# Kernel tuning notes

Measured on AMD Instinct MI355X. Metric: run time of the kernel, lower is better.

Reference implementation:

```python
import jax, jax.numpy as jnp
import numpy as np

B, S, H, NH, L = 8, 512, 768, 12, 12
D = H // NH
EPS = 1e-12


def setup_inputs() -> dict:
    key = jax.random.key(0)
    ks = jax.random.split(key, 16)
    sc = 0.02
    inp = {
        "x": jax.random.normal(ks[0], (B, S, H), dtype=jnp.float32),
        # stacked per-layer params, leading dim L
        "Wq": jax.random.normal(ks[1], (L, H, H), dtype=jnp.float32) * sc,
        "bq": jnp.zeros((L, H), dtype=jnp.float32),
        "Wk": jax.random.normal(ks[2], (L, H, H), dtype=jnp.float32) * sc,
        "bk": jnp.zeros((L, H), dtype=jnp.float32),
        "Wv": jax.random.normal(ks[3], (L, H, H), dtype=jnp.float32) * sc,
        "bv": jnp.zeros((L, H), dtype=jnp.float32),
        "Wo": jax.random.normal(ks[4], (L, H, H), dtype=jnp.float32) * sc,
        "bo": jnp.zeros((L, H), dtype=jnp.float32),
        "ln1_g": jnp.ones((L, H), dtype=jnp.float32),
        "ln1_b": jnp.zeros((L, H), dtype=jnp.float32),
        # NOTE: original code applies pff2 (hidden->hidden, relu) TWICE; pff1 is unused.
        "W2": jax.random.normal(ks[5], (L, H, H), dtype=jnp.float32) * sc,
        "b2": jnp.zeros((L, H), dtype=jnp.float32),
        "ln2_g": jnp.ones((L, H), dtype=jnp.float32),
        "ln2_b": jnp.zeros((L, H), dtype=jnp.float32),
    }
    return inp


def _layernorm(x, g, b):
    m = jnp.mean(x, axis=-1, keepdims=True)
    v = jnp.mean(jnp.square(x - m), axis=-1, keepdims=True)
    return (x - m) * jax.lax.rsqrt(v + EPS) * g + b


def _block(x, p):
    (Wq, bq, Wk, bk, Wv, bv, Wo, bo, g1, be1, W2, b2, g2, be2) = p
    # projections: [B,S,H] -> [B,NH,S,D]
    def split(t):
        return t.reshape(B, S, NH, D).transpose(0, 2, 1, 3)
    q = split(x @ Wq + bq)
    k = split(x @ Wk + bk)
    v = split(x @ Wv + bv)
    scores = jnp.einsum("bhqd,bhkd->bhqk", q, k) / jnp.sqrt(jnp.float32(D))
    att = jax.nn.softmax(scores, axis=-1)  # no mask: original passes mask into `training` slot
    ctx = jnp.einsum("bhqk,bhkd->bhqd", att, v)
    ctx = ctx.transpose(0, 2, 1, 3).reshape(B, S, H)
    attn_out = ctx @ Wo + bo
    out1 = _layernorm(x + attn_out, g1, be1)
    # faithful bug replication: pff2 applied twice, pff1 unused
    h = jax.nn.relu(out1 @ W2 + b2)
    h = jax.nn.relu(h @ W2 + b2)
    out2 = _layernorm(out1 + h, g2, be2)
    return out2


def reference(x, Wq, bq, Wk, bk, Wv, bv, Wo, bo, ln1_g, ln1_b, W2, b2, ln2_g, ln2_b):
    params = (Wq, bq, Wk, bk, Wv, bv, Wo, bo, ln1_g, ln1_b, W2, b2, ln2_g, ln2_b)

    def step(carry, p):
        return _block(carry, p), None

    out, _ = jax.lax.scan(step, x, params)
    return out
```

## Files before the change

kernel.cpp:

```cpp
#include <hip/hip_runtime.h>
#include <cstdint>

typedef __bf16 bf16;
typedef __attribute__((ext_vector_type(4))) __bf16 bf16x4;
typedef __attribute__((ext_vector_type(8))) __bf16 bf16x8;
typedef __attribute__((ext_vector_type(4))) float f32x4;

#define ASYNC16(gptr, lptr)                                                      \
  __builtin_amdgcn_global_load_lds(                                              \
      (const __attribute__((address_space(1))) unsigned int*)(gptr),             \
      (__attribute__((address_space(3))) unsigned int*)(lptr), 16, 0, 0)

template <int BM, int BN, bool BIAS, bool RELU, int RESMODE, bool OUTB, bool VTOUT>
__global__ __launch_bounds__(256) void gemm_bt(
    const bf16* __restrict__ A, const bf16* __restrict__ B, void* __restrict__ C,
    const float* __restrict__ bias, const float* __restrict__ res,
    bf16* __restrict__ vt, int K,
    int lda, int ldb, int ldc, int bdiv, long sA1, long sA2, long sB1, long sB2,
    long sC1, long sC2, float scale)
{
  constexpr int FM = BM / 32, FN = BN / 32;
  constexpr int CALLS_A = BM / 64, CALLS_B = BN / 64;
  __shared__ __align__(16) bf16 As[2 * BM * 32];
  __shared__ __align__(16) bf16 Bs[2 * BN * 32];
  const int tid = threadIdx.x;
  const int wave = tid >> 6, lane = tid & 63;
  const int zb = blockIdx.z / bdiv, zh = blockIdx.z % bdiv;
  const bf16* Ab = A + zb * sA1 + zh * sA2 + (long)blockIdx.y * BM * lda;
  const bf16* Bb = B + zb * sB1 + zh * sB2 + (long)blockIdx.x * BN * ldb;
  const int rA = lane >> 2, kA = (lane & 3) * 8;
  const int wm = wave >> 1, wn = wave & 1;
  const int mBase = wm * (BM / 2) + (lane & 15);
  const int nBase = wn * (BN / 2) + (lane & 15);
  const int kOff = (lane >> 4) * 8;

  f32x4 acc[FM][FN] = {};

  for (int k0 = 0; k0 < K; k0 += 64) {
#pragma unroll
    for (int hh = 0; hh < 2; ++hh) {
      const int kh = k0 + hh * 32;
#pragma unroll
      for (int c = 0; c < CALLS_A; ++c) {
        const int cb = (wave * CALLS_A + c) << 10;
        ASYNC16(Ab + (long)((cb >> 6) + rA) * lda + kh + kA,
                ((char*)As) + hh * (BM * 64) + cb);
      }
#pragma unroll
      for (int c = 0; c < CALLS_B; ++c) {
        const int cb = (wave * CALLS_B + c) << 10;
        ASYNC16(Bb + (long)((cb >> 6) + rA) * ldb + kh + kA,
                ((char*)Bs) + hh * (BN * 64) + cb);
      }
    }
    __syncthreads();
#pragma unroll
    for (int t = 0; t < 2; ++t) {
      const bf16* Asub = As + t * BM * 32;
      const bf16* Bsub = Bs + t * BN * 32;
      bf16x8 af[FM], bfr[FN];
#pragma unroll
      for (int i = 0; i < FM; ++i)
        af[i] = *(const bf16x8*)&Asub[(mBase + i * 16) * 32 + kOff];
#pragma unroll
      for (int j = 0; j < FN; ++j)
        bfr[j] = *(const bf16x8*)&Bsub[(nBase + j * 16) * 32 + kOff];
#pragma unroll
      for (int i = 0; i < FM; ++i)
#pragma unroll
        for (int j = 0; j < FN; ++j)
          acc[i][j] = __builtin_amdgcn_mfma_f32_16x16x32_bf16(af[i], bfr[j], acc[i][j], 0, 0, 0);
    }
    __syncthreads();
  }

  const long cBase = zb * sC1 + zh * sC2;
  const int rowB = blockIdx.y * BM + wm * (BM / 2) + ((lane >> 4) << 2);
  const int colB = blockIdx.x * BN + wn * (BN / 2) + (lane & 15);
#pragma unroll
  for (int i = 0; i < FM; ++i) {
    const int row0 = rowB + i * 16;
#pragma unroll
    for (int j = 0; j < FN; ++j) {
      const int col = colB + j * 16;
      float bv = 0.f;
      if constexpr (BIAS) bv = bias[col];
      bf16x4 pk;
#pragma unroll
      for (int r = 0; r < 4; ++r) {
        const int row = row0 + r;
        float v = acc[i][j][r] * scale + bv;
        if constexpr (RELU) v = fmaxf(v, 0.f);
        const long idx = cBase + (long)row * ldc + col;
        if constexpr (RESMODE == 1) v += res[idx];
        if constexpr (OUTB) ((bf16*)C)[idx] = (bf16)v;
        else                ((float*)C)[idx] = v;
        if constexpr (VTOUT) pk[r] = (bf16)v;
      }
      if constexpr (VTOUT) {
        if (col >= 1536) {
          const int cc = col - 1536;
          const int h = cc >> 6, d = cc & 63;
          const int b = row0 >> 9, s = row0 & 511;
          *(bf16x4*)&vt[(((long)(b * 12 + h) * 64 + d) << 9) + s] = pk;
        }
      }
    }
  }
}

__global__ __launch_bounds__(512, 1) void fattn(
    const bf16* __restrict__ qkv, const bf16* __restrict__ vT,
    bf16* __restrict__ ctx)
{
  __shared__ __align__(16) bf16 Qs[64 * 64];
  __shared__ __align__(16) bf16 KVs[512 * 64];
  __shared__ __align__(16) bf16 Ps[64 * 520];
  __shared__ float sm[64 * 4];
  __shared__ float ssum[64 * 4];

  const int tid = threadIdx.x, wave = tid >> 6, lane = tid & 63;
  const int wg = wave >> 2, wc = wave & 3;
  const int bh = blockIdx.y;
  const int b = bh / 12, h = bh % 12;
  const int q0 = blockIdx.x * 64;
  const bf16* Qg = qkv + (long)(b * 512 + q0) * 2304 + h * 64;
  const bf16* Kg = qkv + (long)(b * 512) * 2304 + 768 + h * 64;
  const bf16* Vg = vT + (long)bh * 32768;

  const int rq = lane >> 3;
  const int kx = (((lane & 7) ^ rq) << 3);
  ASYNC16(Qg + (long)(wave * 8 + rq) * 2304 + kx, ((char*)Qs) + (wave << 10));
#pragma unroll
  for (int c = 0; c < 8; ++c) {
    const int cb = (wave * 8 + c) << 10;
    ASYNC16(Kg + (long)((cb >> 7) + rq) * 2304 + kx, ((char*)KVs) + cb);
  }
  __syncthreads();

  const int m0 = lane & 15, q = lane >> 4;
  const int sw = (m0 & 7);
  f32x4 acc[2][8] = {};
#pragma unroll
  for (int t = 0; t < 2; ++t) {
    const int ch = ((t * 4 + q) ^ sw) << 3;
    bf16x8 af[2];
#pragma unroll
    for (int i = 0; i < 2; ++i)
      af[i] = *(const bf16x8*)&Qs[(wg * 32 + i * 16 + m0) * 64 + ch];
#pragma unroll
    for (int j = 0; j < 8; ++j) {
      bf16x8 bf = *(const bf16x8*)&KVs[(wc * 128 + j * 16 + m0) * 64 + ch];
#pragma unroll
      for (int i = 0; i < 2; ++i)
        acc[i][j] = __builtin_amdgcn_mfma_f32_16x16x32_bf16(af[i], bf, acc[i][j], 0, 0, 0);
    }
  }

#pragma unroll
  for (int i = 0; i < 2; ++i)
#pragma unroll
    for (int r = 0; r < 4; ++r) {
      float m = acc[i][0][r];
#pragma unroll
      for (int j = 1; j < 8; ++j) m = fmaxf(m, acc[i][j][r]);
#pragma unroll
      for (int msk = 1; msk < 16; msk <<= 1) m = fmaxf(m, __shfl_xor(m, msk));
      if (m0 == 0) sm[(wg * 32 + i * 16 + q * 4 + r) * 4 + wc] = m;
    }
  __syncthreads();

  {
#pragma unroll
    for (int c = 0; c < 8; ++c) {
      const int d = wave * 8 + c;
      const int cb = (wave * 8 + c) << 10;
      ASYNC16(Vg + (long)d * 512 + ((lane ^ c) << 3), ((char*)KVs) + cb);
    }
  }

  const float SCL = 0.125f;
#pragma unroll
  for (int i = 0; i < 2; ++i)
#pragma unroll
    for (int r = 0; r < 4; ++r) {
      const int row = wg * 32 + i * 16 + q * 4 + r;
      f32x4 mv = *(const f32x4*)&sm[row * 4];
      const float M = fmaxf(fmaxf(mv[0], mv[1]), fmaxf(mv[2], mv[3])) * SCL;
      float s = 0.f;
#pragma unroll
      for (int j = 0; j < 8; ++j) {
        const float p = __expf(acc[i][j][r] * SCL - M);
        s += p;
        Ps[row * 520 + wc * 128 + j * 16 + m0] = (bf16)p;
      }
#pragma unroll
      for (int msk = 1; msk < 16; msk <<= 1) s += __shfl_xor(s, msk);
      if (m0 == 0) ssum[row * 4 + wc] = s;
    }
  __syncthreads();

  f32x4 cacc[2] = {};
#pragma unroll
  for (int t = 0; t < 16; ++t) {
    const int ch = ((t * 4 + q) ^ sw) << 3;
    bf16x8 bf = *(const bf16x8*)&KVs[(wc * 16 + m0) * 512 + ch];
#pragma unroll
    for (int i = 0; i < 2; ++i) {
      bf16x8 af = *(const bf16x8*)&Ps[(wg * 32 + i * 16 + m0) * 520 + t * 32 + q * 8];
      cacc[i] = __builtin_amdgcn_mfma_f32_16x16x32_bf16(af, bf, cacc[i], 0, 0, 0);
    }
  }
  const long cbase = (long)(b * 512 + q0) * 768 + h * 64;
  const int col = wc * 16 + m0;
#pragma unroll
  for (int i = 0; i < 2; ++i)
#pragma unroll
    for (int r = 0; r < 4; ++r) {
      const int row = wg * 32 + i * 16 + q * 4 + r;
      f32x4 sv = *(const f32x4*)&ssum[row * 4];
      const float inv = 1.f / (sv[0] + sv[1] + sv[2] + sv[3]);
      ctx[cbase + (long)row * 768 + col] = (bf16)(cacc[i][r] * inv);
    }
}

__global__ __launch_bounds__(256) void wprep(
    const float* __restrict__ Wq, const float* __restrict__ Wk,
    const float* __restrict__ Wv, const float* __restrict__ Wo,
    const float* __restrict__ W2, bf16* __restrict__ Tqkv, bf16* __restrict__ To,
    bf16* __restrict__ T2)
{
  const int l = blockIdx.z / 5, t = blockIdx.z % 5;
  const int k0 = blockIdx.x * 64, n0 = blockIdx.y * 64;
  const float* W = (t == 0) ? Wq : (t == 1) ? Wk : (t == 2) ? Wv : (t == 3) ? Wo : W2;
  W += (long)l * 589824;
  __shared__ __align__(16) bf16 tile[64][72];
  const int tid = threadIdx.x;
  const int r = tid >> 2, c = (tid & 3) * 16;
  const float* src = W + (long)(k0 + r) * 768 + n0 + c;
  bf16x8 s0, s1;
#pragma unroll
  for (int i = 0; i < 2; ++i) {
    f32x4 v0 = *(const f32x4*)(src + i * 8);
    f32x4 v1 = *(const f32x4*)(src + i * 8 + 4);
    bf16x8& dstv = i ? s1 : s0;
#pragma unroll
    for (int qq = 0; qq < 4; ++qq) { dstv[qq] = (bf16)v0[qq]; dstv[qq + 4] = (bf16)v1[qq]; }
  }
  *(bf16x8*)&tile[r][c] = s0;
  *(bf16x8*)&tile[r][c + 8] = s1;
  __syncthreads();
  bf16x8 o0, o1;
#pragma unroll
  for (int i = 0; i < 8; ++i) { o0[i] = tile[c + i][r]; o1[i] = tile[c + 8 + i][r]; }
  bf16* dst;
  if (t < 3)       dst = Tqkv + (long)l * 2304 * 768 + (long)(t * 768 + n0 + r) * 768 + k0 + c;
  else if (t == 3) dst = To + (long)l * 589824 + (long)(n0 + r) * 768 + k0 + c;
  else             dst = T2 + (long)l * 589824 + (long)(n0 + r) * 768 + k0 + c;
  *(bf16x8*)dst = o0;
  *(bf16x8*)(dst + 8) = o1;
}

__global__ void bias_concat(const float* __restrict__ bq, const float* __restrict__ bk,
                            const float* __restrict__ bv, float* __restrict__ o)
{
  const int i = blockIdx.x * 256 + threadIdx.x;
  if (i >= 12 * 2304) return;
  const int l = i / 2304, n = i % 2304;
  o[i] = (n < 768) ? bq[l * 768 + n] : (n < 1536) ? bk[l * 768 + n - 768] : bv[l * 768 + n - 1536];
}

__global__ void xconv(const float* __restrict__ x, float* __restrict__ xf, bf16* __restrict__ xb)
{
  const long i = (long)blockIdx.x * 256 + threadIdx.x;
  const float v = x[i];
  xf[i] = v;
  xb[i] = (bf16)v;
}

__global__ __launch_bounds__(256) void layernorm_k(
    const float* __restrict__ in, const float* __restrict__ g,
    const float* __restrict__ b, float* __restrict__ outf, bf16* __restrict__ outb)
{
  const long row = blockIdx.x;
  const int tid = threadIdx.x;
  const float* xr = in + row * 768;
  const float v0 = xr[tid], v1 = xr[tid + 256], v2 = xr[tid + 512];
  float s = v0 + v1 + v2;
  float qv = v0 * v0 + v1 * v1 + v2 * v2;
#pragma unroll
  for (int o = 32; o > 0; o >>= 1) { s += __shfl_down(s, o); qv += __shfl_down(qv, o); }
  __shared__ float rs[4], rq[4];
  const int wave = tid >> 6, lane = tid & 63;
  if (lane == 0) { rs[wave] = s; rq[wave] = qv; }
  __syncthreads();
  const float st = rs[0] + rs[1] + rs[2] + rs[3];
  const float qt = rq[0] + rq[1] + rq[2] + rq[3];
  const float mean = st * (1.f / 768.f);
  float var = qt * (1.f / 768.f) - mean * mean;
  var = fmaxf(var, 0.f);
  const float rstd = rsqrtf(var + 1e-12f);
  const float y0 = (v0 - mean) * rstd * g[tid] + b[tid];
  const float y1 = (v1 - mean) * rstd * g[tid + 256] + b[tid + 256];
  const float y2 = (v2 - mean) * rstd * g[tid + 512] + b[tid + 512];
  float* of = outf + row * 768;
  bf16* ob = outb + row * 768;
  of[tid] = y0;        of[tid + 256] = y1;        of[tid + 512] = y2;
  ob[tid] = (bf16)y0;  ob[tid + 256] = (bf16)y1;  ob[tid + 512] = (bf16)y2;
}

extern "C" void kernel_launch(void* const* d_in, const int* in_sizes, int n_in,
                              void* d_out, int out_size, void* d_ws, size_t ws_size,
                              hipStream_t stream)
{
  const float* x   = (const float*)d_in[0];
  const float* Wq  = (const float*)d_in[1];
  const float* bq  = (const float*)d_in[2];
  const float* Wk  = (const float*)d_in[3];
  const float* bk  = (const float*)d_in[4];
  const float* Wv  = (const float*)d_in[5];
  const float* bv  = (const float*)d_in[6];
  const float* Wo  = (const float*)d_in[7];
  const float* bo  = (const float*)d_in[8];
  const float* g1  = (const float*)d_in[9];
  const float* be1 = (const float*)d_in[10];
  const float* W2  = (const float*)d_in[11];
  const float* b2  = (const float*)d_in[12];
  const float* g2  = (const float*)d_in[13];
  const float* be2 = (const float*)d_in[14];
  (void)in_sizes; (void)n_in; (void)out_size; (void)ws_size;

  char* ws = (char*)d_ws;
  size_t off = 0;
  auto alloc = [&](size_t bytes) {
    void* p = ws + off;
    off = (off + bytes + 255) & ~(size_t)255;
    return p;
  };
  bf16*  wTqkv = (bf16*)alloc(12L * 2304 * 768 * 2);
  bf16*  wTo   = (bf16*)alloc(12L * 768 * 768 * 2);
  bf16*  wT2   = (bf16*)alloc(12L * 768 * 768 * 2);
  float* bqkv  = (float*)alloc(12L * 2304 * 4);
  float* xf    = (float*)alloc(4096L * 768 * 4);
  bf16*  xb    = (bf16*)alloc(4096L * 768 * 2);
  bf16*  qkv   = (bf16*)alloc(4096L * 2304 * 2);
  bf16*  vT    = (bf16*)alloc(96L * 64 * 512 * 2);
  bf16*  ctx   = (bf16*)alloc(4096L * 768 * 2);
  float* res1  = (float*)alloc(4096L * 768 * 4);
  float* out1f = (float*)alloc(4096L * 768 * 4);
  bf16*  out1b = (bf16*)alloc(4096L * 768 * 2);
  bf16*  h1b   = (bf16*)alloc(4096L * 768 * 2);
  float* res2  = (float*)alloc(4096L * 768 * 4);

  wprep<<<dim3(12, 12, 60), 256, 0, stream>>>(Wq, Wk, Wv, Wo, W2, wTqkv, wTo, wT2);
  bias_concat<<<dim3(108), 256, 0, stream>>>(bq, bk, bv, bqkv);
  xconv<<<dim3(12288), 256, 0, stream>>>(x, xf, xb);

  for (int l = 0; l < 12; ++l) {
    const bf16* wq_l   = wTqkv + (long)l * 2304 * 768;
    const bf16* wo_l   = wTo + (long)l * 589824;
    const bf16* w2_l   = wT2 + (long)l * 589824;
    const float* bqk_l = bqkv + l * 2304;
    float* lnout = (l == 11) ? (float*)d_out : xf;

    gemm_bt<128, 128, true, false, 0, true, true><<<dim3(18, 32, 1), 256, 0, stream>>>(
        xb, wq_l, qkv, bqk_l, nullptr, vT, 768, 768, 768, 2304,
        1, 0, 0, 0, 0, 0, 0, 1.f);
    fattn<<<dim3(8, 96), 512, 0, stream>>>(qkv, vT, ctx);
    gemm_bt<128, 64, true, false, 1, false, false><<<dim3(12, 32, 1), 256, 0, stream>>>(
        ctx, wo_l, res1, bo + l * 768, xf, nullptr, 768, 768, 768, 768,
        1, 0, 0, 0, 0, 0, 0, 1.f);
    layernorm_k<<<dim3(4096), 256, 0, stream>>>(res1, g1 + l * 768, be1 + l * 768, out1f, out1b);
    gemm_bt<128, 64, true, true, 0, true, false><<<dim3(12, 32, 1), 256, 0, stream>>>(
        out1b, w2_l, h1b, b2 + l * 768, nullptr, nullptr, 768, 768, 768, 768,
        1, 0, 0, 0, 0, 0, 0, 1.f);
    gemm_bt<128, 64, true, true, 1, false, false><<<dim3(12, 32, 1), 256, 0, stream>>>(
        h1b, w2_l, res2, b2 + l * 768, out1f, nullptr, 768, 768, 768, 768,
        1, 0, 0, 0, 0, 0, 0, 1.f);
    layernorm_k<<<dim3(4096), 256, 0, stream>>>(res2, g2 + l * 768, be2 + l * 768, lnout, xb);
  }
}
```

Measured before the change: 1.728 ms.

## Recompute LayerNorm residual in GEMM epilogue from row stats; rewrite weight transpose

New measurement: 1.710 ms. No clear change (-1.0%).

```diff
diff --git a/kernel.cpp b/kernel.cpp
--- a/kernel.cpp
+++ b/kernel.cpp
@@ -5,6 +5,7 @@
 typedef __attribute__((ext_vector_type(4))) __bf16 bf16x4;
 typedef __attribute__((ext_vector_type(8))) __bf16 bf16x8;
 typedef __attribute__((ext_vector_type(4))) float f32x4;
+typedef __attribute__((ext_vector_type(2))) float f32x2;
 
 #define ASYNC16(gptr, lptr)                                                      \
   __builtin_amdgcn_global_load_lds(                                              \
@@ -15,7 +16,8 @@
 __global__ __launch_bounds__(256) void gemm_bt(
     const bf16* __restrict__ A, const bf16* __restrict__ B, void* __restrict__ C,
     const float* __restrict__ bias, const float* __restrict__ res,
-    bf16* __restrict__ vt, int K,
+    const f32x2* __restrict__ stats, const float* __restrict__ lng,
+    const float* __restrict__ lnb, bf16* __restrict__ vt, int K,
     int lda, int ldb, int ldc, int bdiv, long sA1, long sA2, long sB1, long sB2,
     long sC1, long sC2, float scale)
 {
@@ -85,6 +87,8 @@
       const int col = colB + j * 16;
       float bv = 0.f;
       if constexpr (BIAS) bv = bias[col];
+      float gv = 0.f, lv = 0.f;
+      if constexpr (RESMODE == 3) { gv = lng[col]; lv = lnb[col]; }
       bf16x4 pk;
 #pragma unroll
       for (int r = 0; r < 4; ++r) {
@@ -93,6 +97,10 @@
         if constexpr (RELU) v = fmaxf(v, 0.f);
         const long idx = cBase + (long)row * ldc + col;
         if constexpr (RESMODE == 1) v += res[idx];
+        if constexpr (RESMODE == 3) {
+          const f32x2 st = stats[row];
+          v += (res[idx] - st.x) * st.y * gv + lv;
+        }
         if constexpr (OUTB) ((bf16*)C)[idx] = (bf16)v;
         else                ((float*)C)[idx] = v;
         if constexpr (VTOUT) pk[r] = (bf16)v;
@@ -224,41 +232,69 @@
     }
 }
 
+static __device__ inline unsigned pk2(float lo, float hi) {
+  const unsigned short a = __builtin_bit_cast(unsigned short, (bf16)lo);
+  const unsigned short b = __builtin_bit_cast(unsigned short, (bf16)hi);
+  return (unsigned)a | ((unsigned)b << 16);
+}
+
 __global__ __launch_bounds__(256) void wprep(
     const float* __restrict__ Wq, const float* __restrict__ Wk,
     const float* __restrict__ Wv, const float* __restrict__ Wo,
     const float* __restrict__ W2, bf16* __restrict__ Tqkv, bf16* __restrict__ To,
     bf16* __restrict__ T2)
 {
-  const int l = blockIdx.z / 5, t = blockIdx.z % 5;
-  const int k0 = blockIdx.x * 64, n0 = blockIdx.y * 64;
+  const int l = blockIdx.y / 5, t = blockIdx.y % 5;
+  const int k0 = blockIdx.x * 64;
   const float* W = (t == 0) ? Wq : (t == 1) ? Wk : (t == 2) ? Wv : (t == 3) ? Wo : W2;
   W += (long)l * 589824;
-  __shared__ __align__(16) bf16 tile[64][72];
+  __shared__ unsigned Tl[768 * 34];
   const int tid = threadIdx.x;
-  const int r = tid >> 2, c = (tid & 3) * 16;
-  const float* src = W + (long)(k0 + r) * 768 + n0 + c;
-  bf16x8 s0, s1;
-#pragma unroll
-  for (int i = 0; i < 2; ++i) {
-    f32x4 v0 = *(const f32x4*)(src + i * 8);
-    f32x4 v1 = *(const f32x4*)(src + i * 8 + 4);
-    bf16x8& dstv = i ? s1 : s0;
-#pragma unroll
-    for (int qq = 0; qq < 4; ++qq) { dstv[qq] = (bf16)v0[qq]; dstv[qq + 4] = (bf16)v1[qq]; }
-  }
-  *(bf16x8*)&tile[r][c] = s0;
-  *(bf16x8*)&tile[r][c + 8] = s1;
+
+#pragma unroll
+  for (int it = 0; it < 12; ++it) {
+    const int idx = it * 256 + tid;
+    const int g = idx % 96;
+    const int p = idx / 96;
+    const float* src0 = W + (long)(k0 + 2 * p) * 768 + g * 8;
+    const f32x4 a0 = *(const f32x4*)(src0);
+    const f32x4 a1 = *(const f32x4*)(src0 + 4);
+    const f32x4 b0 = *(const f32x4*)(src0 + 768);
+    const f32x4 b1 = *(const f32x4*)(src0 + 772);
+    const int pc = p ^ (4 * (g & 7));
+    unsigned* rowp = &Tl[(8 * g) * 34];
+#pragma unroll
+    for (int c = 0; c < 4; ++c) {
+      rowp[c * 34 + pc]       = pk2(a0[c], b0[c]);
+      rowp[(c + 4) * 34 + pc] = pk2(a1[c], b1[c]);
+    }
+  }
   __syncthreads();
-  bf16x8 o0, o1;
-#pragma unroll
-  for (int i = 0; i < 8; ++i) { o0[i] = tile[c + i][r]; o1[i] = tile[c + 8 + i][r]; }
-  bf16* dst;
-  if (t < 3)       dst = Tqkv + (long)l * 2304 * 768 + (long)(t * 768 + n0 + r) * 768 + k0 + c;
-  else if (t == 3) dst = To + (long)l * 589824 + (long)(n0 + r) * 768 + k0 + c;
-  else             dst = T2 + (long)l * 589824 + (long)(n0 + r) * 768 + k0 + c;
-  *(bf16x8*)dst = o0;
-  *(bf16x8*)(dst + 8) = o1;
+
+  bf16* dstBase;
+  if (t < 3)       dstBase = Tqkv + (long)l * 2304 * 768 + (long)t * 768 * 768;
+  else if (t == 3) dstBase = To + (long)l * 589824;
+  else             dstBase = T2 + (long)l * 589824;
+
+#pragma unroll
+  for (int it = 0; it < 12; ++it) {
+    const int n = it * 64 + (tid >> 2);
+    const int q = tid & 3;
+    const int key = 4 * ((n >> 3) & 7);
+    const unsigned* row = &Tl[n * 34];
+    unsigned o[8];
+#pragma unroll
+    for (int i = 0; i < 4; ++i) {
+      const int col = (8 * q + 2 * i) ^ key;
+      const uint2 u = *(const uint2*)&row[col];
+      o[2 * i] = u.x; o[2 * i + 1] = u.y;
+    }
+    unsigned* d = (unsigned*)(dstBase + (long)n * 768 + k0) + q * 8;
+    uint4 w0; w0.x = o[0]; w0.y = o[1]; w0.z = o[2]; w0.w = o[3];
+    uint4 w1; w1.x = o[4]; w1.y = o[5]; w1.z = o[6]; w1.w = o[7];
+    *(uint4*)d = w0;
+    *(uint4*)(d + 4) = w1;
+  }
 }
 
 __global__ void bias_concat(const float* __restrict__ bq, const float* __restrict__ bk,
@@ -270,17 +306,16 @@
   o[i] = (n < 768) ? bq[l * 768 + n] : (n < 1536) ? bk[l * 768 + n - 768] : bv[l * 768 + n - 1536];
 }
 
-__global__ void xconv(const float* __restrict__ x, float* __restrict__ xf, bf16* __restrict__ xb)
+__global__ void xconv(const float* __restrict__ x, bf16* __restrict__ xb)
 {
   const long i = (long)blockIdx.x * 256 + threadIdx.x;
-  const float v = x[i];
-  xf[i] = v;
-  xb[i] = (bf16)v;
+  xb[i] = (bf16)x[i];
 }
 
 __global__ __launch_bounds__(256) void layernorm_k(
     const float* __restrict__ in, const float* __restrict__ g,
-    const float* __restrict__ b, float* __restrict__ outf, bf16* __restrict__ outb)
+    const float* __restrict__ b, bf16* __restrict__ outb,
+    f32x2* __restrict__ stats, float* __restrict__ outf)
 {
   const long row = blockIdx.x;
   const int tid = threadIdx.x;
@@ -300,13 +335,16 @@
   float var = qt * (1.f / 768.f) - mean * mean;
   var = fmaxf(var, 0.f);
   const float rstd = rsqrtf(var + 1e-12f);
+  if (tid == 0) { f32x2 sv; sv.x = mean; sv.y = rstd; stats[row] = sv; }
   const float y0 = (v0 - mean) * rstd * g[tid] + b[tid];
   const float y1 = (v1 - mean) * rstd * g[tid + 256] + b[tid + 256];
   const float y2 = (v2 - mean) * rstd * g[tid + 512] + b[tid + 512];
-  float* of = outf + row * 768;
   bf16* ob = outb + row * 768;
-  of[tid] = y0;        of[tid + 256] = y1;        of[tid + 512] = y2;
-  ob[tid] = (bf16)y0;  ob[tid + 256] = (bf16)y1;  ob[tid + 512] = (bf16)y2;
+  ob[tid] = (bf16)y0; ob[tid + 256] = (bf16)y1; ob[tid + 512] = (bf16)y2;
+  if (outf) {
+    float* of = outf + row * 768;
+    of[tid] = y0; of[tid + 256] = y1; of[tid + 512] = y2;
+  }
 }
 
 extern "C" void kernel_launch(void* const* d_in, const int* in_sizes, int n_in,
@@ -337,46 +375,55 @@
     off = (off + bytes + 255) & ~(size_t)255;
     return p;
   };
-  bf16*  wTqkv = (bf16*)alloc(12L * 2304 * 768 * 2);
-  bf16*  wTo   = (bf16*)alloc(12L * 768 * 768 * 2);
-  bf16*  wT2   = (bf16*)alloc(12L * 768 * 768 * 2);
-  float* bqkv  = (float*)alloc(12L * 2304 * 4);
-  float* xf    = (float*)alloc(4096L * 768 * 4);
-  bf16*  xb    = (bf16*)alloc(4096L * 768 * 2);
-  bf16*  qkv   = (bf16*)alloc(4096L * 2304 * 2);
-  bf16*  vT    = (bf16*)alloc(96L * 64 * 512 * 2);
-  bf16*  ctx   = (bf16*)alloc(4096L * 768 * 2);
-  float* res1  = (float*)alloc(4096L * 768 * 4);
-  float* out1f = (float*)alloc(4096L * 768 * 4);
-  bf16*  out1b = (bf16*)alloc(4096L * 768 * 2);
-  bf16*  h1b   = (bf16*)alloc(4096L * 768 * 2);
-  float* res2  = (float*)alloc(4096L * 768 * 4);
-
-  wprep<<<dim3(12, 12, 60), 256, 0, stream>>>(Wq, Wk, Wv, Wo, W2, wTqkv, wTo, wT2);
+  bf16*  wTqkv  = (bf16*)alloc(12L * 2304 * 768 * 2);
+  bf16*  wTo    = (bf16*)alloc(12L * 768 * 768 * 2);
+  bf16*  wT2    = (bf16*)alloc(12L * 768 * 768 * 2);
+  float* bqkv   = (float*)alloc(12L * 2304 * 4);
+  bf16*  xb     = (bf16*)alloc(4096L * 768 * 2);
+  bf16*  qkv    = (bf16*)alloc(4096L * 2304 * 2);
+  bf16*  vT     = (bf16*)alloc(96L * 64 * 512 * 2);
+  bf16*  ctx    = (bf16*)alloc(4096L * 768 * 2);
+  float* res1   = (float*)alloc(4096L * 768 * 4);
+  bf16*  out1b  = (bf16*)alloc(4096L * 768 * 2);
+  bf16*  h1b    = (bf16*)alloc(4096L * 768 * 2);
+  float* res2   = (float*)alloc(4096L * 768 * 4);
+  f32x2* stats1 = (f32x2*)alloc(4096L * 8);
+  f32x2* stats2 = (f32x2*)alloc(4096L * 8);
+
+  wprep<<<dim3(12, 60), 256, 0, stream>>>(Wq, Wk, Wv, Wo, W2, wTqkv, wTo, wT2);
   bias_concat<<<dim3(108), 256, 0, stream>>>(bq, bk, bv, bqkv);
-  xconv<<<dim3(12288), 256, 0, stream>>>(x, xf, xb);
+  xconv<<<dim3(12288), 256, 0, stream>>>(x, xb);
 
   for (int l = 0; l < 12; ++l) {
     const bf16* wq_l   = wTqkv + (long)l * 2304 * 768;
     const bf16* wo_l   = wTo + (long)l * 589824;
     const bf16* w2_l   = wT2 + (long)l * 589824;
     const float* bqk_l = bqkv + l * 2304;
-    float* lnout = (l == 11) ? (float*)d_out : xf;
 
     gemm_bt<128, 128, true, false, 0, true, true><<<dim3(18, 32, 1), 256, 0, stream>>>(
-        xb, wq_l, qkv, bqk_l, nullptr, vT, 768, 768, 768, 2304,
-        1, 0, 0, 0, 0, 0, 0, 1.f);
+        xb, wq_l, qkv, bqk_l, nullptr, nullptr, nullptr, nullptr, vT, 768,
+        768, 768, 2304, 1, 0, 0, 0, 0, 0, 0, 1.f);
     fattn<<<dim3(8, 96), 512, 0, stream>>>(qkv, vT, ctx);
-    gemm_bt<128, 64, true, false, 1, false, false><<<dim3(12, 32, 1), 256, 0, stream>>>(
-        ctx, wo_l, res1, bo + l * 768, xf, nullptr, 768, 768, 768, 768,
-        1, 0, 0, 0, 0, 0, 0, 1.f);
-    layernorm_k<<<dim3(4096), 256, 0, stream>>>(res1, g1 + l * 768, be1 + l * 768, out1f, out1b);
+    if (l == 0) {
+      gemm_bt<128, 64, true, false, 1, false, false><<<dim3(12, 32, 1), 256, 0, stream>>>(
+          ctx, wo_l, res1, bo, x, nullptr, nullptr, nullptr, nullptr, 768,
+          768, 768, 768, 1, 0, 0, 0, 0, 0, 0, 1.f);
+    } else {
+      gemm_bt<128, 64, true, false, 3, false, false><<<dim3(12, 32, 1), 256, 0, stream>>>(
+          ctx, wo_l, res1, bo + l * 768, res2, stats2,
+          g2 + (l - 1) * 768, be2 + (l - 1) * 768, nullptr, 768,
+          768, 768, 768, 1, 0, 0, 0, 0, 0, 0, 1.f);
+    }
+    layernorm_k<<<dim3(4096), 256, 0, stream>>>(res1, g1 + l * 768, be1 + l * 768,
+                                                out1b, stats1, nullptr);
     gemm_bt<128, 64, true, true, 0, true, false><<<dim3(12, 32, 1), 256, 0, stream>>>(
-        out1b, w2_l, h1b, b2 + l * 768, nullptr, nullptr, 768, 768, 768, 768,
-        1, 0, 0, 0, 0, 0, 0, 1.f);
-    gemm_bt<128, 64, true, true, 1, false, false><<<dim3(12, 32, 1), 256, 0, stream>>>(
-        h1b, w2_l, res2, b2 + l * 768, out1f, nullptr, 768, 768, 768, 768,
-        1, 0, 0, 0, 0, 0, 0, 1.f);
-    layernorm_k<<<dim3(4096), 256, 0, stream>>>(res2, g2 + l * 768, be2 + l * 768, lnout, xb);
-  }
-}
+        out1b, w2_l, h1b, b2 + l * 768, nullptr, nullptr, nullptr, nullptr, nullptr, 768,
+        768, 768, 768, 1, 0, 0, 0, 0, 0, 0, 1.f);
+    gemm_bt<128, 64, true, true, 3, false, false><<<dim3(12, 32, 1), 256, 0, stream>>>(
+        h1b, w2_l, res2, b2 + l * 768, res1, stats1,
+        g1 + l * 768, be1 + l * 768, nullptr, 768,
+        768, 768, 768, 1, 0, 0, 0, 0, 0, 0, 1.f);
+    layernorm_k<<<dim3(4096), 256, 0, stream>>>(res2, g2 + l * 768, be2 + l * 768,
+                                                xb, stats2, (l == 11) ? (float*)d_out : nullptr);
+  }
+}
```
